# Optimization experiments

Measured on AMD Instinct MI355X. Metric: run time of the kernel, lower is better.

The kernel has to match this reference:

```python
import jax, jax.numpy as jnp
import numpy as np

B, H, KLEN, D = 32, 8, 8192, 64  # batch, heads, kv_len, head_dim


def setup_inputs() -> dict:
    key = jax.random.key(0)
    k1, k2, k3, k4 = jax.random.split(key, 4)
    std = 1.0 / D ** 0.5
    Q = jax.random.normal(k1, (B, H, 1, D), dtype=jnp.float32)
    K = jax.random.normal(k2, (B, H, KLEN, D), dtype=jnp.float32)
    W_c = jax.random.normal(k3, (H, 2 * D, D), dtype=jnp.float32) * std
    W_o = jax.random.normal(k4, (H, D, 1), dtype=jnp.float32) * std
    bias = jnp.zeros((H, 1, D), dtype=jnp.float32)
    return {"Q": Q, "K": K, "W_c": W_c, "W_o": W_o, "bias": bias}


def reference(Q, K, W_c, W_o, bias):
    # concat score (NAIS, He et al. 2018)
    Qe = jnp.broadcast_to(Q, K.shape)                       # [b,h,k,d]
    QK_cat = jnp.concatenate([Qe, K], axis=-1)              # [b,h,k,2d]
    hidden = jax.nn.relu(
        jnp.einsum('bhke,hed->bhkd', QK_cat, W_c) + bias    # bias [h,1,d] broadcasts
    )                                                        # [b,h,k,d]
    scores = jnp.einsum('bhkd,hde->bhk', hidden, W_o)       # sums over d and e(=1)
    return scores
```

## Files before the change

kernel.cpp:

```cpp
#include <hip/hip_runtime.h>
#include <stdint.h>

#define B_    32
#define H_    8
#define KLEN_ 8192
#define D_    64
#define SPLIT 16
#define ROWS_PER_BLOCK (KLEN_ / SPLIT)
#define WAVES 4
#define TILES (ROWS_PER_BLOCK / (WAVES * 16))

#define LDS_ROW 144

typedef __attribute__((ext_vector_type(8))) short short8;
typedef __attribute__((ext_vector_type(4))) float float4v;
typedef __attribute__((ext_vector_type(4))) unsigned int uint4v;
typedef __attribute__((ext_vector_type(2))) unsigned int uint2v;

static __device__ inline unsigned int pack_bf16(float x0, float x1) {
    unsigned int a = __builtin_bit_cast(unsigned int, x0) + 0x8000u;
    unsigned int b = __builtin_bit_cast(unsigned int, x1) + 0x8000u;
    return __builtin_amdgcn_perm(b, a, 0x07060302u);
}

__global__ __launch_bounds__(256) void nais_score_kernel(
    const float* __restrict__ Q,
    const float* __restrict__ K,
    const float* __restrict__ Wc,
    const float* __restrict__ Wo,
    const float* __restrict__ bias,
    float* __restrict__ out)
{
    const int blk   = blockIdx.x;
    const int bh    = blk / SPLIT;
    const int split = blk % SPLIT;
    const int h     = bh % H_;
    const int tid   = threadIdx.x;
    const int lane  = tid & 63;
    const int wave  = tid >> 6;
    const int c     = lane & 15;
    const int q     = lane >> 4;

    __shared__ float s_qb[D_];
    __shared__ float s_wo[D_];
    __shared__ unsigned char s_tile[WAVES][16 * LDS_ROW] __attribute__((aligned(16)));

    if (tid < D_) {
        const float* qv = Q + (size_t)bh * D_;
        const float* wq = Wc + (size_t)h * (2 * D_ * D_);
        float acc = bias[h * D_ + tid];
        #pragma unroll 8
        for (int e = 0; e < D_; ++e)
            acc += qv[e] * wq[e * D_ + tid];
        s_qb[tid] = acc;
        s_wo[tid] = Wo[h * D_ + tid];
    }
    __syncthreads();

    const float* wk = Wc + (size_t)h * (2 * D_ * D_) + D_ * D_;
    short8 bfrag[4][2];
    #pragma unroll
    for (int t = 0; t < 4; ++t) {
        const int d = t * 16 + c;
        #pragma unroll
        for (int half = 0; half < 2; ++half) {
            uint4v f;
            #pragma unroll
            for (int j2 = 0; j2 < 4; ++j2) {
                const int e = half * 32 + q * 8 + 2 * j2;
                f[j2] = pack_bf16(wk[(size_t)e * D_ + d], wk[(size_t)(e + 1) * D_ + d]);
            }
            bfrag[t][half] = __builtin_bit_cast(short8, f);
        }
    }

    float qbl[4], wol[4];
    #pragma unroll
    for (int t = 0; t < 4; ++t) {
        qbl[t] = s_qb[t * 16 + c];
        wol[t] = s_wo[t * 16 + c];
    }

    const float* Kb = K + (size_t)bh * KLEN_ * D_ + (size_t)split * ROWS_PER_BLOCK * D_;
    float*       ob = out + (size_t)bh * KLEN_ + (size_t)split * ROWS_PER_BLOCK;
    unsigned char* myTile = s_tile[wave];

    #define TILE_PTR(t) (Kb + (size_t)(((t) * WAVES + wave) * 16) * D_)

    float4v st[2][4];
    #pragma unroll
    for (int j = 0; j < 4; ++j)
        st[0][j] = *(const float4v*)(TILE_PTR(0) + j * 256 + lane * 4);

    for (int t = 0; t < TILES; ++t) {
        const int cb = t & 1, nb = cb ^ 1;
        if (t + 1 < TILES) {
            #pragma unroll
            for (int j = 0; j < 4; ++j)
                st[nb][j] = *(const float4v*)(TILE_PTR(t + 1) + j * 256 + lane * 4);
        }

        #pragma unroll
        for (int j = 0; j < 4; ++j) {
            const int r = j * 4 + q;
            uint2v w;
            w[0] = pack_bf16(st[cb][j][0], st[cb][j][1]);
            w[1] = pack_bf16(st[cb][j][2], st[cb][j][3]);
            *(uint2v*)(myTile + r * LDS_ROW + c * 8) = w;
        }

        short8 af0 = *(const short8*)(myTile + c * LDS_ROW + q * 16);
        short8 af1 = *(const short8*)(myTile + c * LDS_ROW + 64 + q * 16);

        float4v pr = {0.f, 0.f, 0.f, 0.f};
        #pragma unroll
        for (int tt = 0; tt < 4; ++tt) {
            float4v acc = {0.f, 0.f, 0.f, 0.f};
            acc = __builtin_amdgcn_mfma_f32_16x16x32_bf16(af0, bfrag[tt][0], acc, 0, 0, 0);
            acc = __builtin_amdgcn_mfma_f32_16x16x32_bf16(af1, bfrag[tt][1], acc, 0, 0, 0);
            #pragma unroll
            for (int r = 0; r < 4; ++r) {
                float hv = fmaxf(acc[r] + qbl[tt], 0.f);
                pr[r] += hv * wol[tt];
            }
        }

        const int krow = (t * WAVES + wave) * 16;
        #pragma unroll
        for (int r = 0; r < 4; ++r) {
            float v = pr[r];
            v += __shfl_xor(v, 1);
            v += __shfl_xor(v, 2);
            v += __shfl_xor(v, 4);
            v += __shfl_xor(v, 8);
            if (c == r) ob[krow + q * 4 + r] = v;
        }
    }
    #undef TILE_PTR
}

extern "C" void kernel_launch(void* const* d_in, const int* in_sizes, int n_in,
                              void* d_out, int out_size, void* d_ws, size_t ws_size,
                              hipStream_t stream) {
    const float* Q    = (const float*)d_in[0];
    const float* K    = (const float*)d_in[1];
    const float* Wc   = (const float*)d_in[2];
    const float* Wo   = (const float*)d_in[3];
    const float* bias = (const float*)d_in[4];
    float* out = (float*)d_out;

    dim3 grid(B_ * H_ * SPLIT);
    dim3 block(256);
    nais_score_kernel<<<grid, block, 0, stream>>>(Q, K, Wc, Wo, bias, out);
}
```

Measured before the change: 692.7 us.

## Load K fragments directly into registers and swap MFMA operands to drop LDS staging

Each lane now loads its own K row slice straight from global memory in the MFMA B-operand layout, removing the per-tile LDS write/read transpose. The MFMA operands are swapped (W as A, K as B), so hidden dims land along the accumulator rows and the per-row reduction needs only two cross-lane shuffles instead of sixteen. The global loads become less coalesced per instruction (strided 16-byte chunks across rows), which may cost memory efficiency on this bandwidth-bound kernel.

After: 695.0 us. Within noise of the previous version (+0.3%).

```diff
diff --git a/kernel.cpp b/kernel.cpp
--- a/kernel.cpp
+++ b/kernel.cpp
@@ -10,17 +10,23 @@
 #define WAVES 4
 #define TILES (ROWS_PER_BLOCK / (WAVES * 16))
 
-#define LDS_ROW 144
-
 typedef __attribute__((ext_vector_type(8))) short short8;
 typedef __attribute__((ext_vector_type(4))) float float4v;
 typedef __attribute__((ext_vector_type(4))) unsigned int uint4v;
-typedef __attribute__((ext_vector_type(2))) unsigned int uint2v;
 
 static __device__ inline unsigned int pack_bf16(float x0, float x1) {
     unsigned int a = __builtin_bit_cast(unsigned int, x0) + 0x8000u;
     unsigned int b = __builtin_bit_cast(unsigned int, x1) + 0x8000u;
     return __builtin_amdgcn_perm(b, a, 0x07060302u);
+}
+
+static __device__ inline short8 pack8(const float4v& lo, const float4v& hi) {
+    uint4v u;
+    u[0] = pack_bf16(lo[0], lo[1]);
+    u[1] = pack_bf16(lo[2], lo[3]);
+    u[2] = pack_bf16(hi[0], hi[1]);
+    u[3] = pack_bf16(hi[2], hi[3]);
+    return __builtin_bit_cast(short8, u);
 }
 
 __global__ __launch_bounds__(256) void nais_score_kernel(
@@ -43,7 +49,6 @@
 
     __shared__ float s_qb[D_];
     __shared__ float s_wo[D_];
-    __shared__ unsigned char s_tile[WAVES][16 * LDS_ROW] __attribute__((aligned(16)));
 
     if (tid < D_) {
         const float* qv = Q + (size_t)bh * D_;
@@ -58,7 +63,7 @@
     __syncthreads();
 
     const float* wk = Wc + (size_t)h * (2 * D_ * D_) + D_ * D_;
-    short8 bfrag[4][2];
+    short8 wfrag[4][2];
     #pragma unroll
     for (int t = 0; t < 4; ++t) {
         const int d = t * 16 + c;
@@ -70,73 +75,65 @@
                 const int e = half * 32 + q * 8 + 2 * j2;
                 f[j2] = pack_bf16(wk[(size_t)e * D_ + d], wk[(size_t)(e + 1) * D_ + d]);
             }
-            bfrag[t][half] = __builtin_bit_cast(short8, f);
+            wfrag[t][half] = __builtin_bit_cast(short8, f);
         }
     }
 
-    float qbl[4], wol[4];
+    float qbl[4][4], wol[4][4];
     #pragma unroll
-    for (int t = 0; t < 4; ++t) {
-        qbl[t] = s_qb[t * 16 + c];
-        wol[t] = s_wo[t * 16 + c];
-    }
+    for (int t = 0; t < 4; ++t)
+        #pragma unroll
+        for (int r = 0; r < 4; ++r) {
+            qbl[t][r] = s_qb[t * 16 + q * 4 + r];
+            wol[t][r] = s_wo[t * 16 + q * 4 + r];
+        }
 
     const float* Kb = K + (size_t)bh * KLEN_ * D_ + (size_t)split * ROWS_PER_BLOCK * D_;
     float*       ob = out + (size_t)bh * KLEN_ + (size_t)split * ROWS_PER_BLOCK;
-    unsigned char* myTile = s_tile[wave];
 
-    #define TILE_PTR(t) (Kb + (size_t)(((t) * WAVES + wave) * 16) * D_)
+    #define ROW_PTR(t) (Kb + (size_t)((((t) * WAVES + wave) * 16) + c) * D_ + q * 8)
 
-    float4v st[2][4];
-    #pragma unroll
-    for (int j = 0; j < 4; ++j)
-        st[0][j] = *(const float4v*)(TILE_PTR(0) + j * 256 + lane * 4);
+    float4v st[4];
+    {
+        const float* p = ROW_PTR(0);
+        st[0] = *(const float4v*)(p);
+        st[1] = *(const float4v*)(p + 4);
+        st[2] = *(const float4v*)(p + 32);
+        st[3] = *(const float4v*)(p + 36);
+    }
 
     for (int t = 0; t < TILES; ++t) {
-        const int cb = t & 1, nb = cb ^ 1;
+        short8 af0 = pack8(st[0], st[1]);
+        short8 af1 = pack8(st[2], st[3]);
+
         if (t + 1 < TILES) {
-            #pragma unroll
-            for (int j = 0; j < 4; ++j)
-                st[nb][j] = *(const float4v*)(TILE_PTR(t + 1) + j * 256 + lane * 4);
+            const float* p = ROW_PTR(t + 1);
+            st[0] = *(const float4v*)(p);
+            st[1] = *(const float4v*)(p + 4);
+            st[2] = *(const float4v*)(p + 32);
+            st[3] = *(const float4v*)(p + 36);
         }
 
-        #pragma unroll
-        for (int j = 0; j < 4; ++j) {
-            const int r = j * 4 + q;
-            uint2v w;
-            w[0] = pack_bf16(st[cb][j][0], st[cb][j][1]);
-            w[1] = pack_bf16(st[cb][j][2], st[cb][j][3]);
-            *(uint2v*)(myTile + r * LDS_ROW + c * 8) = w;
-        }
-
-        short8 af0 = *(const short8*)(myTile + c * LDS_ROW + q * 16);
-        short8 af1 = *(const short8*)(myTile + c * LDS_ROW + 64 + q * 16);
-
-        float4v pr = {0.f, 0.f, 0.f, 0.f};
+        float pr = 0.f;
         #pragma unroll
         for (int tt = 0; tt < 4; ++tt) {
             float4v acc = {0.f, 0.f, 0.f, 0.f};
-            acc = __builtin_amdgcn_mfma_f32_16x16x32_bf16(af0, bfrag[tt][0], acc, 0, 0, 0);
-            acc = __builtin_amdgcn_mfma_f32_16x16x32_bf16(af1, bfrag[tt][1], acc, 0, 0, 0);
+            acc = __builtin_amdgcn_mfma_f32_16x16x32_bf16(wfrag[tt][0], af0, acc, 0, 0, 0);
+            acc = __builtin_amdgcn_mfma_f32_16x16x32_bf16(wfrag[tt][1], af1, acc, 0, 0, 0);
             #pragma unroll
             for (int r = 0; r < 4; ++r) {
-                float hv = fmaxf(acc[r] + qbl[tt], 0.f);
-                pr[r] += hv * wol[tt];
+                float hv = fmaxf(acc[r] + qbl[tt][r], 0.f);
+                pr = fmaf(hv, wol[tt][r], pr);
             }
         }
 
+        pr += __shfl_xor(pr, 16);
+        pr += __shfl_xor(pr, 32);
+
         const int krow = (t * WAVES + wave) * 16;
-        #pragma unroll
-        for (int r = 0; r < 4; ++r) {
-            float v = pr[r];
-            v += __shfl_xor(v, 1);
-            v += __shfl_xor(v, 2);
-            v += __shfl_xor(v, 4);
-            v += __shfl_xor(v, 8);
-            if (c == r) ob[krow + q * 4 + r] = v;
-        }
+        if (q == 0) ob[krow + c] = pr;
     }
-    #undef TILE_PTR
+    #undef ROW_PTR
 }
 
 extern "C" void kernel_launch(void* const* d_in, const int* in_sizes, int n_in,
```
